# Optimization experiments

Hardware: AMD Instinct MI355X
Metric: run time of the kernel (lower is better)

The kernel has to match this reference:

```python
import jax, jax.numpy as jnp
import numpy as np

D_MODEL = 16
D_FF = 32
BLOCK = 64
B = 16384
EPS = 1e-5


def setup_inputs() -> dict:
    key = jax.random.key(0)
    ks = jax.random.split(key, 8)
    s = 1.0 / np.sqrt(D_MODEL)
    return {
        "x": jax.random.normal(ks[0], (B, BLOCK, D_MODEL), dtype=jnp.float32),
        # attention projections, stored as [in, out] so y = x @ W
        "Wk": jax.random.uniform(ks[1], (D_MODEL, D_MODEL), jnp.float32, -s, s),
        "Wq": jax.random.uniform(ks[2], (D_MODEL, D_MODEL), jnp.float32, -s, s),
        "Wv": jax.random.uniform(ks[3], (D_MODEL, D_MODEL), jnp.float32, -s, s),
        "ln1_g": jnp.ones((D_MODEL,), jnp.float32),
        "ln1_b": jnp.zeros((D_MODEL,), jnp.float32),
        "ln2_g": jnp.ones((D_MODEL,), jnp.float32),
        "ln2_b": jnp.zeros((D_MODEL,), jnp.float32),
        "W1": jax.random.uniform(ks[4], (D_MODEL, D_FF), jnp.float32, -s, s),
        "b1": jax.random.uniform(ks[5], (D_FF,), jnp.float32, -s, s),
        "W2": jax.random.uniform(ks[6], (D_FF, D_MODEL), jnp.float32, -1/np.sqrt(D_FF), 1/np.sqrt(D_FF)),
        "b2": jax.random.uniform(ks[7], (D_MODEL,), jnp.float32, -1/np.sqrt(D_FF), 1/np.sqrt(D_FF)),
    }


def _layernorm(x, g, b):
    mu = jnp.mean(x, axis=-1, keepdims=True)
    var = jnp.mean(jnp.square(x - mu), axis=-1, keepdims=True)
    return (x - mu) * jax.lax.rsqrt(var + EPS) * g + b


def reference(x, Wk, Wq, Wv, ln1_g, ln1_b, ln2_g, ln2_b, W1, b1, W2, b2):
    B_, T, C = x.shape
    h = _layernorm(x, ln1_g, ln1_b)
    k = h @ Wk
    q = h @ Wq
    v = h @ Wv
    att = jnp.einsum("btc,bsc->bts", q, k) / jnp.sqrt(jnp.float32(C))
    causal = jnp.tril(jnp.ones((T, T), dtype=bool))
    att = jnp.where(causal, att, -jnp.inf)
    att = jax.nn.softmax(att, axis=-1)
    y = jnp.einsum("bts,bsc->btc", att, v)
    x = x + y
    h2 = _layernorm(x, ln2_g, ln2_b)
    ff = jax.nn.gelu(h2 @ W1 + b1, approximate=False) @ W2 + b2
    return x + ff
```

## Files before the change

### kernel.cpp

```cpp
#include <hip/hip_runtime.h>
#include <hip/hip_bf16.h>


typedef __attribute__((ext_vector_type(8))) short bf8;
typedef __attribute__((ext_vector_type(4))) float f4;

union FragU { uint4 u4; uint u[4]; bf8 b; };
union F4U  { uint4 u4; float4 f; };

#define LWAIT() asm volatile("s_waitcnt lgkmcnt(0)" ::: "memory")

__device__ __forceinline__ uint packbf(float lo, float hi) {
    union { __hip_bfloat162 h; uint u; } c;
    c.h = __float22bfloat162_rn(make_float2(lo, hi));
    return c.u;
}

__device__ __forceinline__ float gelu_fast(float u) {
    float u2 = u * u;
    float t  = u * (-2.3022079f + -0.1029431f * u2);
    float e  = __builtin_amdgcn_exp2f(t);
    return u * __builtin_amdgcn_rcpf(1.f + e);
}

#define MFMA(a, b, c) __builtin_amdgcn_mfma_f32_16x16x32_bf16(a, b, c, 0, 0, 0)

#define OQ  0
#define OK  768
#define OV  1536
#define OP  0
#define OH2 0
#define OU  768
#define WARENA 2304
#define NWAVES 4

#define WS_SLOTS 16

__device__ __forceinline__ void loadWfrag(const float* __restrict__ W, int ld,
                                          int n, int kb, bool valid, float scale,
                                          bf8& hf) {
    FragU H;
    if (valid) {
        #pragma unroll
        for (int p = 0; p < 4; ++p)
            H.u[p] = packbf(W[(kb+2*p)*ld+n]*scale, W[(kb+2*p+1)*ld+n]*scale);
    } else {
        H.u4 = make_uint4(0u,0u,0u,0u);
    }
    hf = H.b;
}

__global__ __launch_bounds__(64, 1)
void prep_kernel(const float* __restrict__ Wk, const float* __restrict__ Wq,
                 const float* __restrict__ Wv,
                 const float* __restrict__ ln1g, const float* __restrict__ ln1b,
                 const float* __restrict__ ln2g, const float* __restrict__ ln2b,
                 const float* __restrict__ W1, const float* __restrict__ b1,
                 const float* __restrict__ W2, const float* __restrict__ b2,
                 uint4* __restrict__ ws)
{
    const int lane = threadIdx.x;
    const int c15  = lane & 15;
    const int quad = lane >> 4;
    const int quad4 = quad << 2;
    const bool kv = (quad < 2);
    const int  kb = quad * 8;
    uint4* o = ws + lane * WS_SLOTS;
    FragU t; bf8 f;
    loadWfrag(Wq, 16, c15, kb, kv, 0.25f*1.44269504f, f); t.b = f; o[0] = t.u4;
    loadWfrag(Wk, 16, c15, kb, kv, 1.0f, f);              t.b = f; o[1] = t.u4;
    loadWfrag(Wv, 16, c15, kb, kv, 1.0f, f);              t.b = f; o[2] = t.u4;
    loadWfrag(W1, 32, c15,      kb, kv,   1.0f, f);       t.b = f; o[3] = t.u4;
    loadWfrag(W1, 32, c15 + 16, kb, kv,   1.0f, f);       t.b = f; o[4] = t.u4;
    loadWfrag(W2, 16, c15,      kb, true, 1.0f, f);       t.b = f; o[5] = t.u4;
    F4U z; z.f = make_float4(0.f, 0.f, 0.f, 0.f);
    F4U a, b;
    if (kv) {
        a.f = *(const float4*)(ln1g + kb); b.f = *(const float4*)(ln1g + kb + 4);
    } else { a = z; b = z; }
    o[6] = a.u4; o[7] = b.u4;
    if (kv) {
        a.f = *(const float4*)(ln1b + kb); b.f = *(const float4*)(ln1b + kb + 4);
    } else { a = z; b = z; }
    o[8] = a.u4; o[9] = b.u4;
    a.f = *(const float4*)(ln2g + quad4); o[10] = a.u4;
    a.f = *(const float4*)(ln2b + quad4); o[11] = a.u4;
    a.f = *(const float4*)(b1 + quad4);      o[12] = a.u4;
    a.f = *(const float4*)(b1 + 16 + quad4); o[13] = a.u4;
    a.f = *(const float4*)(b2 + quad4);      o[14] = a.u4;
}

__global__ __launch_bounds__(64 * NWAVES, 4)
void tb_kernel(const float* __restrict__ x,
               const uint4* __restrict__ ws,
               float* __restrict__ out)
{
    __shared__ __align__(16) uint lds_all[NWAVES * WARENA];
    const int tid  = threadIdx.x;
    const int lane = tid & 63;
    const int wid  = tid >> 6;
    uint* __restrict__ lds = lds_all + wid * WARENA;
    const int c15  = lane & 15;
    const int quad = lane >> 4;
    const int quad4 = quad << 2;
    const size_t base = (size_t)(blockIdx.x * NWAVES + wid) * (64 * 16);
    const f4 z4 = {0.f, 0.f, 0.f, 0.f};
    const bool kv = (quad < 2);
    const int  kb = quad * 8;
    const bool wrE = ((c15 & 1) == 0);

    float4 xr[4];
    #pragma unroll
    for (int qt = 0; qt < 4; ++qt)
        xr[qt] = *(const float4*)(x + base + (size_t)(qt*16 + c15)*16 + quad4);

    const uint4* wv = ws + lane * WS_SLOTS;
    FragU t;
    t.u4 = wv[0]; const bf8 fWq  = t.b;
    t.u4 = wv[1]; const bf8 fWk  = t.b;
    t.u4 = wv[2]; const bf8 fWv  = t.b;
    t.u4 = wv[3]; const bf8 fW1a = t.b;
    t.u4 = wv[4]; const bf8 fW1b = t.b;
    t.u4 = wv[5]; const bf8 fW2f = t.b;
    F4U fu;
    fu.u4 = wv[6];  const float4 g1a = fu.f;
    fu.u4 = wv[7];  const float4 g1b = fu.f;
    fu.u4 = wv[8];  const float4 b1a = fu.f;
    fu.u4 = wv[9];  const float4 b1b = fu.f;
    fu.u4 = wv[10]; const float4 g2  = fu.f;
    fu.u4 = wv[11]; const float4 b2v = fu.f;
    fu.u4 = wv[12]; const f4 cb0 = {fu.f.x, fu.f.y, fu.f.z, fu.f.w};
    fu.u4 = wv[13]; const f4 cb1 = {fu.f.x, fu.f.y, fu.f.z, fu.f.w};
    fu.u4 = wv[14]; const f4 cb2 = {fu.f.x, fu.f.y, fu.f.z, fu.f.w};

    bf8 ah[4];
    {
        const float gg[8] = {g1a.x,g1a.y,g1a.z,g1a.w, g1b.x,g1b.y,g1b.z,g1b.w};
        const float bb[8] = {b1a.x,b1a.y,b1a.z,b1a.w, b1b.x,b1b.y,b1b.z,b1b.w};
        #pragma unroll
        for (int mt = 0; mt < 4; ++mt) {
            FragU Ah;
            if (kv) {
                const float4* xp = (const float4*)(x + base + (size_t)(mt*16 + c15)*16 + kb);
                float4 v0 = xp[0], v1 = xp[1];
                float xv[8] = {v0.x,v0.y,v0.z,v0.w, v1.x,v1.y,v1.z,v1.w};
                float s = 0.f;
                #pragma unroll
                for (int j = 0; j < 8; ++j) s += xv[j];
                s  += __shfl_xor(s, 16);
                float mu = s * 0.0625f;
                float s2 = 0.f;
                #pragma unroll
                for (int j = 0; j < 8; ++j) { float d = xv[j] - mu; s2 += d*d; }
                s2 += __shfl_xor(s2, 16);
                float var  = s2 * 0.0625f;
                float rstd = rsqrtf(var + 1e-5f);
                float h[8];
                #pragma unroll
                for (int j = 0; j < 8; ++j) h[j] = (xv[j]-mu)*rstd*gg[j] + bb[j];
                #pragma unroll
                for (int p = 0; p < 4; ++p) Ah.u[p] = packbf(h[2*p], h[2*p+1]);
            } else {
                Ah.u4 = make_uint4(0u,0u,0u,0u);
            }
            ah[mt] = Ah.b;
        }
    }

    #pragma unroll
    for (int mt = 0; mt < 4; ++mt) {
        f4 qc = MFMA(ah[mt], fWq, z4);
        f4 kc = MFMA(ah[mt], fWk, z4);
        f4 vc = MFMA(ah[mt], fWv, z4);
        #pragma unroll
        for (int r = 0; r < 4; ++r) {
            const int tok = mt*16 + quad4 + r;
            float qo = __shfl_xor(qc[r], 1);
            float ko = __shfl_xor(kc[r], 1);
            if (wrE) {
                lds[OQ + tok*12 + (c15>>1)] = packbf(qc[r], qo);
                lds[OK + tok*12 + (c15>>1)] = packbf(kc[r], ko);
            }
        }
        *(uint2*)(lds + OV + c15*36 + mt*8 + quad*2) =
            make_uint2(packbf(vc[0], vc[1]), packbf(vc[2], vc[3]));
    }
    LWAIT();

    bf8 qb[4];
    #pragma unroll
    for (int qt = 0; qt < 4; ++qt) {
        FragU H;
        if (kv) H.u4 = *(const uint4*)(lds + OQ + (qt*16 + c15)*12 + quad4);
        else    H.u4 = make_uint4(0u,0u,0u,0u);
        qb[qt] = H.b;
    }
    f4 st[4][4];
    #pragma unroll
    for (int kt = 0; kt < 4; ++kt) {
        FragU H;
        if (kv) H.u4 = *(const uint4*)(lds + OK + (kt*16 + c15)*12 + quad4);
        else    H.u4 = make_uint4(0u,0u,0u,0u);
        bf8 ka = H.b;
        #pragma unroll
        for (int qt = 3; qt >= 0; --qt)
            if (qt >= kt)
                st[kt][qt] = MFMA(ka, qb[qt], z4);
    }
    #pragma unroll
    for (int qt = 0; qt < 4; ++qt)
        #pragma unroll
        for (int r = 0; r < 4; ++r)
            st[qt][qt][r] = (quad4 + r <= c15) ? st[qt][qt][r] : -1e30f;

    float linv[4];
    #pragma unroll
    for (int qt = 0; qt < 4; ++qt) {
        float mx = fmaxf(fmaxf(st[0][qt][0], st[0][qt][1]),
                         fmaxf(st[0][qt][2], st[0][qt][3]));
        #pragma unroll
        for (int kt = 1; kt < 4; ++kt) {
            if (kt <= qt) {
                float mk = fmaxf(fmaxf(st[kt][qt][0], st[kt][qt][1]),
                                 fmaxf(st[kt][qt][2], st[kt][qt][3]));
                mx = fmaxf(mx, mk);
            }
        }
        mx = fmaxf(mx, __shfl_xor(mx, 16));
        mx = fmaxf(mx, __shfl_xor(mx, 32));
        float l = 0.f;
        #pragma unroll
        for (int kt = 0; kt < 4; ++kt) {
            if (kt <= qt) {
                #pragma unroll
                for (int r = 0; r < 4; ++r) {
                    float p = __builtin_amdgcn_exp2f(st[kt][qt][r] - mx);
                    st[kt][qt][r] = p;
                    l += p;
                }
            }
        }
        l += __shfl_xor(l, 16);
        l += __shfl_xor(l, 32);
        linv[qt] = __builtin_amdgcn_rcpf(l);
    }

    bf8 va[2];
    #pragma unroll
    for (int kc = 0; kc < 2; ++kc) {
        FragU H;
        H.u4 = *(const uint4*)(lds + OV + c15*36 + kc*16 + quad4);
        va[kc] = H.b;
    }
    LWAIT();

    #pragma unroll
    for (int qt = 0; qt < 4; ++qt) {
        const int rowo = OP + (qt*16 + c15)*36 + quad*2;
        #pragma unroll
        for (int kt = 0; kt < 4; ++kt) {
            uint2 w;
            if (kt <= qt) {
                w.x = packbf(st[kt][qt][0], st[kt][qt][1]);
                w.y = packbf(st[kt][qt][2], st[kt][qt][3]);
            } else w = make_uint2(0u, 0u);
            *(uint2*)(lds + rowo + kt*8) = w;
        }
    }
    LWAIT();

    f4 yt[4];
    #pragma unroll
    for (int qt = 0; qt < 4; ++qt) {
        f4 acc = z4;
        #pragma unroll
        for (int kc = 0; kc < 2; ++kc) {
            if (kc == 0 || qt >= 2) {
                FragU P_;
                P_.u4 = *(const uint4*)(lds + OP + (qt*16 + c15)*36 + kc*16 + quad4);
                acc = MFMA(va[kc], P_.b, acc);
            }
        }
        yt[qt] = acc;
    }

    float x2v[4][4];
    #pragma unroll
    for (int qt = 0; qt < 4; ++qt) {
        const float li = linv[qt];
        x2v[qt][0] = xr[qt].x + yt[qt][0]*li;
        x2v[qt][1] = xr[qt].y + yt[qt][1]*li;
        x2v[qt][2] = xr[qt].z + yt[qt][2]*li;
        x2v[qt][3] = xr[qt].w + yt[qt][3]*li;
    }
    LWAIT();

    #pragma unroll
    for (int qt = 0; qt < 4; ++qt) {
        float s = x2v[qt][0]+x2v[qt][1]+x2v[qt][2]+x2v[qt][3];
        s += __shfl_xor(s, 16); s += __shfl_xor(s, 32);
        float mu = s * 0.0625f;
        float d0 = x2v[qt][0]-mu, d1 = x2v[qt][1]-mu,
              d2 = x2v[qt][2]-mu, d3 = x2v[qt][3]-mu;
        float s2 = d0*d0 + d1*d1 + d2*d2 + d3*d3;
        s2 += __shfl_xor(s2, 16); s2 += __shfl_xor(s2, 32);
        float rstd = rsqrtf(s2 * 0.0625f + 1e-5f);
        float h0 = d0*rstd*g2.x + b2v.x;
        float h1 = d1*rstd*g2.y + b2v.y;
        float h2_ = d2*rstd*g2.z + b2v.z;
        float h3 = d3*rstd*g2.w + b2v.w;
        *(uint2*)(lds + OH2 + (qt*16 + c15)*12 + quad*2) =
            make_uint2(packbf(h0, h1), packbf(h2_, h3));
    }
    LWAIT();

    f4 uu[2][4];
    #pragma unroll
    for (int qt = 0; qt < 4; ++qt) {
        FragU H;
        if (kv) H.u4 = *(const uint4*)(lds + OH2 + (qt*16 + c15)*12 + quad4);
        else    H.u4 = make_uint4(0u,0u,0u,0u);
        uu[0][qt] = MFMA(fW1a, H.b, cb0);
        uu[1][qt] = MFMA(fW1b, H.b, cb1);
    }
    #pragma unroll
    for (int qt = 0; qt < 4; ++qt) {
        const int row = OU + (qt*16 + c15)*20;
        #pragma unroll
        for (int nt = 0; nt < 2; ++nt) {
            float e0 = gelu_fast(uu[nt][qt][0]);
            float e1 = gelu_fast(uu[nt][qt][1]);
            float e2 = gelu_fast(uu[nt][qt][2]);
            float e3 = gelu_fast(uu[nt][qt][3]);
            *(uint2*)(lds + row + nt*8 + quad*2) =
                make_uint2(packbf(e0, e1), packbf(e2, e3));
        }
    }
    LWAIT();

    #pragma unroll
    for (int qt = 0; qt < 4; ++qt) {
        FragU H;
        H.u4 = *(const uint4*)(lds + OU + (qt*16 + c15)*20 + quad4);
        f4 fo = MFMA(fW2f, H.b, cb2);
        float4 o;
        o.x = x2v[qt][0] + fo[0];
        o.y = x2v[qt][1] + fo[1];
        o.z = x2v[qt][2] + fo[2];
        o.w = x2v[qt][3] + fo[3];
        *(float4*)(out + base + (size_t)(qt*16 + c15)*16 + quad4) = o;
    }
}

extern "C" void kernel_launch(void* const* d_in, const int* in_sizes, int n_in,
                              void* d_out, int out_size, void* d_ws, size_t ws_size,
                              hipStream_t stream) {
    const float* x     = (const float*)d_in[0];
    const float* Wk    = (const float*)d_in[1];
    const float* Wq    = (const float*)d_in[2];
    const float* Wv    = (const float*)d_in[3];
    const float* ln1_g = (const float*)d_in[4];
    const float* ln1_b = (const float*)d_in[5];
    const float* ln2_g = (const float*)d_in[6];
    const float* ln2_b = (const float*)d_in[7];
    const float* W1    = (const float*)d_in[8];
    const float* b1    = (const float*)d_in[9];
    const float* W2    = (const float*)d_in[10];
    const float* b2    = (const float*)d_in[11];
    float* out = (float*)d_out;
    uint4* ws = (uint4*)d_ws;

    prep_kernel<<<1, 64, 0, stream>>>(Wk, Wq, Wv, ln1_g, ln1_b, ln2_g, ln2_b,
                                      W1, b1, W2, b2, ws);
    const int n_blocks = in_sizes[0] / (64 * 16);
    const int nwg = n_blocks / NWAVES;
    tb_kernel<<<nwg, 64 * NWAVES, 0, stream>>>(x, ws, out);
}
```

Before: 173.3 us.

## Switch to 16x16x16 bf16 MFMA so fragments stay in registers, bypassing LDS

Replaces the 16x16x32 MFMA, whose K=32 halves were half zero-padded, with the 16x16x16 variant. MFMA output fragments now line up with the next stage's input layout, so V, the probability tiles, the LN2 output and the GELU activations are repacked in registers instead of going through LDS round trips and waits. LN1 now reuses the already-loaded x registers instead of a second global read. The LDS arena shrinks and several lgkmcnt waits are removed, at the cost of issuing more MFMA instructions, for example two for the W2 projection.

New measurement: 152.8 us. 1.13x faster.

```diff
diff --git a/kernel.cpp b/kernel.cpp
--- a/kernel.cpp
+++ b/kernel.cpp
@@ -2,10 +2,10 @@
 #include <hip/hip_bf16.h>
 
 
-typedef __attribute__((ext_vector_type(8))) short bf8;
+typedef __attribute__((ext_vector_type(4))) short bf4;
 typedef __attribute__((ext_vector_type(4))) float f4;
 
-union FragU { uint4 u4; uint u[4]; bf8 b; };
+union Frag2 { uint2 u2; uint u[2]; bf4 b; };
 union F4U  { uint4 u4; float4 f; };
 
 #define LWAIT() asm volatile("s_waitcnt lgkmcnt(0)" ::: "memory")
@@ -23,31 +23,21 @@
     return u * __builtin_amdgcn_rcpf(1.f + e);
 }
 
-#define MFMA(a, b, c) __builtin_amdgcn_mfma_f32_16x16x32_bf16(a, b, c, 0, 0, 0)
+#define MFMA16(a, b, c) __builtin_amdgcn_mfma_f32_16x16x16bf16_1k(a, b, c, 0, 0, 0)
 
 #define OQ  0
-#define OK  768
-#define OV  1536
-#define OP  0
-#define OH2 0
-#define OU  768
-#define WARENA 2304
+#define OK  640
+#define WARENA 1280
 #define NWAVES 4
 
 #define WS_SLOTS 16
 
-__device__ __forceinline__ void loadWfrag(const float* __restrict__ W, int ld,
-                                          int n, int kb, bool valid, float scale,
-                                          bf8& hf) {
-    FragU H;
-    if (valid) {
-        #pragma unroll
-        for (int p = 0; p < 4; ++p)
-            H.u[p] = packbf(W[(kb+2*p)*ld+n]*scale, W[(kb+2*p+1)*ld+n]*scale);
-    } else {
-        H.u4 = make_uint4(0u,0u,0u,0u);
-    }
-    hf = H.b;
+__device__ __forceinline__ uint2 wfrag16(const float* __restrict__ W, int ld,
+                                         int n, int q, float s) {
+    uint2 w;
+    w.x = packbf(W[(q*4+0)*ld+n]*s, W[(q*4+1)*ld+n]*s);
+    w.y = packbf(W[(q*4+2)*ld+n]*s, W[(q*4+3)*ld+n]*s);
+    return w;
 }
 
 __global__ __launch_bounds__(64, 1)
@@ -63,31 +53,26 @@
     const int c15  = lane & 15;
     const int quad = lane >> 4;
     const int quad4 = quad << 2;
-    const bool kv = (quad < 2);
-    const int  kb = quad * 8;
     uint4* o = ws + lane * WS_SLOTS;
-    FragU t; bf8 f;
-    loadWfrag(Wq, 16, c15, kb, kv, 0.25f*1.44269504f, f); t.b = f; o[0] = t.u4;
-    loadWfrag(Wk, 16, c15, kb, kv, 1.0f, f);              t.b = f; o[1] = t.u4;
-    loadWfrag(Wv, 16, c15, kb, kv, 1.0f, f);              t.b = f; o[2] = t.u4;
-    loadWfrag(W1, 32, c15,      kb, kv,   1.0f, f);       t.b = f; o[3] = t.u4;
-    loadWfrag(W1, 32, c15 + 16, kb, kv,   1.0f, f);       t.b = f; o[4] = t.u4;
-    loadWfrag(W2, 16, c15,      kb, true, 1.0f, f);       t.b = f; o[5] = t.u4;
-    F4U z; z.f = make_float4(0.f, 0.f, 0.f, 0.f);
-    F4U a, b;
-    if (kv) {
-        a.f = *(const float4*)(ln1g + kb); b.f = *(const float4*)(ln1g + kb + 4);
-    } else { a = z; b = z; }
-    o[6] = a.u4; o[7] = b.u4;
-    if (kv) {
-        a.f = *(const float4*)(ln1b + kb); b.f = *(const float4*)(ln1b + kb + 4);
-    } else { a = z; b = z; }
-    o[8] = a.u4; o[9] = b.u4;
-    a.f = *(const float4*)(ln2g + quad4); o[10] = a.u4;
-    a.f = *(const float4*)(ln2b + quad4); o[11] = a.u4;
-    a.f = *(const float4*)(b1 + quad4);      o[12] = a.u4;
-    a.f = *(const float4*)(b1 + 16 + quad4); o[13] = a.u4;
-    a.f = *(const float4*)(b2 + quad4);      o[14] = a.u4;
+    uint2 fq  = wfrag16(Wq, 16, c15, quad, 0.25f*1.44269504f);
+    uint2 fk  = wfrag16(Wk, 16, c15, quad, 1.0f);
+    uint2 fv  = wfrag16(Wv, 16, c15, quad, 1.0f);
+    uint2 f1a = wfrag16(W1, 32, c15,      quad, 1.0f);
+    uint2 f1b = wfrag16(W1, 32, c15 + 16, quad, 1.0f);
+    uint2 f2a = wfrag16(W2,        16, c15, quad, 1.0f);
+    uint2 f2b = wfrag16(W2 + 256,  16, c15, quad, 1.0f);
+    o[0] = make_uint4(fq.x, fq.y, fk.x, fk.y);
+    o[1] = make_uint4(fv.x, fv.y, f1a.x, f1a.y);
+    o[2] = make_uint4(f1b.x, f1b.y, f2a.x, f2a.y);
+    o[3] = make_uint4(f2b.x, f2b.y, 0u, 0u);
+    F4U a;
+    a.f = *(const float4*)(ln1g + quad4); o[4]  = a.u4;
+    a.f = *(const float4*)(ln1b + quad4); o[5]  = a.u4;
+    a.f = *(const float4*)(ln2g + quad4); o[6]  = a.u4;
+    a.f = *(const float4*)(ln2b + quad4); o[7]  = a.u4;
+    a.f = *(const float4*)(b1 + quad4);      o[8]  = a.u4;
+    a.f = *(const float4*)(b1 + 16 + quad4); o[9]  = a.u4;
+    a.f = *(const float4*)(b2 + quad4);      o[10] = a.u4;
 }
 
 __global__ __launch_bounds__(64 * NWAVES, 4)
@@ -105,8 +90,6 @@
     const int quad4 = quad << 2;
     const size_t base = (size_t)(blockIdx.x * NWAVES + wid) * (64 * 16);
     const f4 z4 = {0.f, 0.f, 0.f, 0.f};
-    const bool kv = (quad < 2);
-    const int  kb = quad * 8;
     const bool wrE = ((c15 & 1) == 0);
 
     float4 xr[4];
@@ -115,98 +98,83 @@
         xr[qt] = *(const float4*)(x + base + (size_t)(qt*16 + c15)*16 + quad4);
 
     const uint4* wv = ws + lane * WS_SLOTS;
-    FragU t;
-    t.u4 = wv[0]; const bf8 fWq  = t.b;
-    t.u4 = wv[1]; const bf8 fWk  = t.b;
-    t.u4 = wv[2]; const bf8 fWv  = t.b;
-    t.u4 = wv[3]; const bf8 fW1a = t.b;
-    t.u4 = wv[4]; const bf8 fW1b = t.b;
-    t.u4 = wv[5]; const bf8 fW2f = t.b;
+    uint4 s0 = wv[0], s1 = wv[1], s2 = wv[2], s3 = wv[3];
+    Frag2 T;
+    T.u[0]=s0.x; T.u[1]=s0.y; const bf4 fWq  = T.b;
+    T.u[0]=s0.z; T.u[1]=s0.w; const bf4 fWk  = T.b;
+    T.u[0]=s1.x; T.u[1]=s1.y; const bf4 fWv  = T.b;
+    T.u[0]=s1.z; T.u[1]=s1.w; const bf4 fW1a = T.b;
+    T.u[0]=s2.x; T.u[1]=s2.y; const bf4 fW1b = T.b;
+    T.u[0]=s2.z; T.u[1]=s2.w; const bf4 fW2a = T.b;
+    T.u[0]=s3.x; T.u[1]=s3.y; const bf4 fW2b = T.b;
     F4U fu;
-    fu.u4 = wv[6];  const float4 g1a = fu.f;
-    fu.u4 = wv[7];  const float4 g1b = fu.f;
-    fu.u4 = wv[8];  const float4 b1a = fu.f;
-    fu.u4 = wv[9];  const float4 b1b = fu.f;
-    fu.u4 = wv[10]; const float4 g2  = fu.f;
-    fu.u4 = wv[11]; const float4 b2v = fu.f;
-    fu.u4 = wv[12]; const f4 cb0 = {fu.f.x, fu.f.y, fu.f.z, fu.f.w};
-    fu.u4 = wv[13]; const f4 cb1 = {fu.f.x, fu.f.y, fu.f.z, fu.f.w};
-    fu.u4 = wv[14]; const f4 cb2 = {fu.f.x, fu.f.y, fu.f.z, fu.f.w};
-
-    bf8 ah[4];
-    {
-        const float gg[8] = {g1a.x,g1a.y,g1a.z,g1a.w, g1b.x,g1b.y,g1b.z,g1b.w};
-        const float bb[8] = {b1a.x,b1a.y,b1a.z,b1a.w, b1b.x,b1b.y,b1b.z,b1b.w};
-        #pragma unroll
-        for (int mt = 0; mt < 4; ++mt) {
-            FragU Ah;
-            if (kv) {
-                const float4* xp = (const float4*)(x + base + (size_t)(mt*16 + c15)*16 + kb);
-                float4 v0 = xp[0], v1 = xp[1];
-                float xv[8] = {v0.x,v0.y,v0.z,v0.w, v1.x,v1.y,v1.z,v1.w};
-                float s = 0.f;
-                #pragma unroll
-                for (int j = 0; j < 8; ++j) s += xv[j];
-                s  += __shfl_xor(s, 16);
-                float mu = s * 0.0625f;
-                float s2 = 0.f;
-                #pragma unroll
-                for (int j = 0; j < 8; ++j) { float d = xv[j] - mu; s2 += d*d; }
-                s2 += __shfl_xor(s2, 16);
-                float var  = s2 * 0.0625f;
-                float rstd = rsqrtf(var + 1e-5f);
-                float h[8];
-                #pragma unroll
-                for (int j = 0; j < 8; ++j) h[j] = (xv[j]-mu)*rstd*gg[j] + bb[j];
-                #pragma unroll
-                for (int p = 0; p < 4; ++p) Ah.u[p] = packbf(h[2*p], h[2*p+1]);
-            } else {
-                Ah.u4 = make_uint4(0u,0u,0u,0u);
-            }
-            ah[mt] = Ah.b;
-        }
-    }
-
+    fu.u4 = wv[4];  const float4 g1  = fu.f;
+    fu.u4 = wv[5];  const float4 b1l = fu.f;
+    fu.u4 = wv[6];  const float4 g2  = fu.f;
+    fu.u4 = wv[7];  const float4 b2l = fu.f;
+    fu.u4 = wv[8];  const f4 cb0 = {fu.f.x, fu.f.y, fu.f.z, fu.f.w};
+    fu.u4 = wv[9];  const f4 cb1 = {fu.f.x, fu.f.y, fu.f.z, fu.f.w};
+    fu.u4 = wv[10]; const f4 cb2 = {fu.f.x, fu.f.y, fu.f.z, fu.f.w};
+
+    bf4 ah[4];
+    #pragma unroll
+    for (int qt = 0; qt < 4; ++qt) {
+        float4 v = xr[qt];
+        float s = v.x + v.y + v.z + v.w;
+        s += __shfl_xor(s, 16); s += __shfl_xor(s, 32);
+        float mu = s * 0.0625f;
+        float d0 = v.x-mu, d1 = v.y-mu, d2 = v.z-mu, d3 = v.w-mu;
+        float s2 = d0*d0 + d1*d1 + d2*d2 + d3*d3;
+        s2 += __shfl_xor(s2, 16); s2 += __shfl_xor(s2, 32);
+        float rstd = rsqrtf(s2 * 0.0625f + 1e-5f);
+        float h0 = d0*rstd*g1.x + b1l.x;
+        float h1 = d1*rstd*g1.y + b1l.y;
+        float h2 = d2*rstd*g1.z + b1l.z;
+        float h3 = d3*rstd*g1.w + b1l.w;
+        Frag2 A; A.u[0] = packbf(h0, h1); A.u[1] = packbf(h2, h3);
+        ah[qt] = A.b;
+    }
+
+    bf4 va[4];
     #pragma unroll
     for (int mt = 0; mt < 4; ++mt) {
-        f4 qc = MFMA(ah[mt], fWq, z4);
-        f4 kc = MFMA(ah[mt], fWk, z4);
-        f4 vc = MFMA(ah[mt], fWv, z4);
+        f4 qc = MFMA16(ah[mt], fWq, z4);
+        f4 kc = MFMA16(ah[mt], fWk, z4);
+        f4 vc = MFMA16(ah[mt], fWv, z4);
         #pragma unroll
         for (int r = 0; r < 4; ++r) {
             const int tok = mt*16 + quad4 + r;
             float qo = __shfl_xor(qc[r], 1);
             float ko = __shfl_xor(kc[r], 1);
             if (wrE) {
-                lds[OQ + tok*12 + (c15>>1)] = packbf(qc[r], qo);
-                lds[OK + tok*12 + (c15>>1)] = packbf(kc[r], ko);
-            }
-        }
-        *(uint2*)(lds + OV + c15*36 + mt*8 + quad*2) =
-            make_uint2(packbf(vc[0], vc[1]), packbf(vc[2], vc[3]));
+                lds[OQ + tok*10 + (c15>>1)] = packbf(qc[r], qo);
+                lds[OK + tok*10 + (c15>>1)] = packbf(kc[r], ko);
+            }
+        }
+        Frag2 V_;
+        V_.u[0] = packbf(vc[0], vc[1]);
+        V_.u[1] = packbf(vc[2], vc[3]);
+        va[mt] = V_.b;
     }
     LWAIT();
 
-    bf8 qb[4];
-    #pragma unroll
-    for (int qt = 0; qt < 4; ++qt) {
-        FragU H;
-        if (kv) H.u4 = *(const uint4*)(lds + OQ + (qt*16 + c15)*12 + quad4);
-        else    H.u4 = make_uint4(0u,0u,0u,0u);
-        qb[qt] = H.b;
-    }
+    bf4 ka[4], qb[4];
+    #pragma unroll
+    for (int t = 0; t < 4; ++t) {
+        Frag2 A_, B_;
+        A_.u2 = *(const uint2*)(lds + OK + (t*16 + c15)*10 + quad*2);
+        B_.u2 = *(const uint2*)(lds + OQ + (t*16 + c15)*10 + quad*2);
+        ka[t] = A_.b;
+        qb[t] = B_.b;
+    }
+
     f4 st[4][4];
     #pragma unroll
-    for (int kt = 0; kt < 4; ++kt) {
-        FragU H;
-        if (kv) H.u4 = *(const uint4*)(lds + OK + (kt*16 + c15)*12 + quad4);
-        else    H.u4 = make_uint4(0u,0u,0u,0u);
-        bf8 ka = H.b;
+    for (int kt = 0; kt < 4; ++kt)
         #pragma unroll
         for (int qt = 3; qt >= 0; --qt)
             if (qt >= kt)
-                st[kt][qt] = MFMA(ka, qb[qt], z4);
-    }
+                st[kt][qt] = MFMA16(ka[kt], qb[qt], z4);
     #pragma unroll
     for (int qt = 0; qt < 4; ++qt)
         #pragma unroll
@@ -245,46 +213,24 @@
         linv[qt] = __builtin_amdgcn_rcpf(l);
     }
 
-    bf8 va[2];
-    #pragma unroll
-    for (int kc = 0; kc < 2; ++kc) {
-        FragU H;
-        H.u4 = *(const uint4*)(lds + OV + c15*36 + kc*16 + quad4);
-        va[kc] = H.b;
-    }
-    LWAIT();
-
-    #pragma unroll
-    for (int qt = 0; qt < 4; ++qt) {
-        const int rowo = OP + (qt*16 + c15)*36 + quad*2;
+    f4 yt[4];
+    #pragma unroll
+    for (int qt = 0; qt < 4; ++qt) {
+        f4 acc = z4;
         #pragma unroll
         for (int kt = 0; kt < 4; ++kt) {
-            uint2 w;
             if (kt <= qt) {
-                w.x = packbf(st[kt][qt][0], st[kt][qt][1]);
-                w.y = packbf(st[kt][qt][2], st[kt][qt][3]);
-            } else w = make_uint2(0u, 0u);
-            *(uint2*)(lds + rowo + kt*8) = w;
-        }
-    }
-    LWAIT();
-
-    f4 yt[4];
-    #pragma unroll
-    for (int qt = 0; qt < 4; ++qt) {
-        f4 acc = z4;
-        #pragma unroll
-        for (int kc = 0; kc < 2; ++kc) {
-            if (kc == 0 || qt >= 2) {
-                FragU P_;
-                P_.u4 = *(const uint4*)(lds + OP + (qt*16 + c15)*36 + kc*16 + quad4);
-                acc = MFMA(va[kc], P_.b, acc);
+                Frag2 P_;
+                P_.u[0] = packbf(st[kt][qt][0], st[kt][qt][1]);
+                P_.u[1] = packbf(st[kt][qt][2], st[kt][qt][3]);
+                acc = MFMA16(va[kt], P_.b, acc);
             }
         }
         yt[qt] = acc;
     }
 
     float x2v[4][4];
+    f4 uu0[4], uu1[4];
     #pragma unroll
     for (int qt = 0; qt < 4; ++qt) {
         const float li = linv[qt];
@@ -292,11 +238,6 @@
         x2v[qt][1] = xr[qt].y + yt[qt][1]*li;
         x2v[qt][2] = xr[qt].z + yt[qt][2]*li;
         x2v[qt][3] = xr[qt].w + yt[qt][3]*li;
-    }
-    LWAIT();
-
-    #pragma unroll
-    for (int qt = 0; qt < 4; ++qt) {
         float s = x2v[qt][0]+x2v[qt][1]+x2v[qt][2]+x2v[qt][3];
         s += __shfl_xor(s, 16); s += __shfl_xor(s, 32);
         float mu = s * 0.0625f;
@@ -305,44 +246,24 @@
         float s2 = d0*d0 + d1*d1 + d2*d2 + d3*d3;
         s2 += __shfl_xor(s2, 16); s2 += __shfl_xor(s2, 32);
         float rstd = rsqrtf(s2 * 0.0625f + 1e-5f);
-        float h0 = d0*rstd*g2.x + b2v.x;
-        float h1 = d1*rstd*g2.y + b2v.y;
-        float h2_ = d2*rstd*g2.z + b2v.z;
-        float h3 = d3*rstd*g2.w + b2v.w;
-        *(uint2*)(lds + OH2 + (qt*16 + c15)*12 + quad*2) =
-            make_uint2(packbf(h0, h1), packbf(h2_, h3));
-    }
-    LWAIT();
-
-    f4 uu[2][4];
-    #pragma unroll
-    for (int qt = 0; qt < 4; ++qt) {
-        FragU H;
-        if (kv) H.u4 = *(const uint4*)(lds + OH2 + (qt*16 + c15)*12 + quad4);
-        else    H.u4 = make_uint4(0u,0u,0u,0u);
-        uu[0][qt] = MFMA(fW1a, H.b, cb0);
-        uu[1][qt] = MFMA(fW1b, H.b, cb1);
-    }
-    #pragma unroll
-    for (int qt = 0; qt < 4; ++qt) {
-        const int row = OU + (qt*16 + c15)*20;
-        #pragma unroll
-        for (int nt = 0; nt < 2; ++nt) {
-            float e0 = gelu_fast(uu[nt][qt][0]);
-            float e1 = gelu_fast(uu[nt][qt][1]);
-            float e2 = gelu_fast(uu[nt][qt][2]);
-            float e3 = gelu_fast(uu[nt][qt][3]);
-            *(uint2*)(lds + row + nt*8 + quad*2) =
-                make_uint2(packbf(e0, e1), packbf(e2, e3));
-        }
-    }
-    LWAIT();
-
-    #pragma unroll
-    for (int qt = 0; qt < 4; ++qt) {
-        FragU H;
-        H.u4 = *(const uint4*)(lds + OU + (qt*16 + c15)*20 + quad4);
-        f4 fo = MFMA(fW2f, H.b, cb2);
+        float h0 = d0*rstd*g2.x + b2l.x;
+        float h1 = d1*rstd*g2.y + b2l.y;
+        float h2 = d2*rstd*g2.z + b2l.z;
+        float h3 = d3*rstd*g2.w + b2l.w;
+        Frag2 Hb;
+        Hb.u[0] = packbf(h0, h1); Hb.u[1] = packbf(h2, h3);
+        uu0[qt] = MFMA16(fW1a, Hb.b, cb0);
+        uu1[qt] = MFMA16(fW1b, Hb.b, cb1);
+    }
+    #pragma unroll
+    for (int qt = 0; qt < 4; ++qt) {
+        Frag2 Pa, Pb;
+        Pa.u[0] = packbf(gelu_fast(uu0[qt][0]), gelu_fast(uu0[qt][1]));
+        Pa.u[1] = packbf(gelu_fast(uu0[qt][2]), gelu_fast(uu0[qt][3]));
+        Pb.u[0] = packbf(gelu_fast(uu1[qt][0]), gelu_fast(uu1[qt][1]));
+        Pb.u[1] = packbf(gelu_fast(uu1[qt][2]), gelu_fast(uu1[qt][3]));
+        f4 fo = MFMA16(fW2a, Pa.b, cb2);
+        fo = MFMA16(fW2b, Pb.b, fo);
         float4 o;
         o.x = x2v[qt][0] + fo[0];
         o.y = x2v[qt][1] + fo[1];
```
